# Performance work log

Measured on AMD Instinct MI355X. Metric: run time of the kernel, lower is better.

The kernel has to match this reference:

```python
import jax, jax.numpy as jnp
import numpy as np

N_PTS = 1048576
N_SPHERES = 128
K_SMOOTH = 32.0
CLAMP_MIN = 1e-6


def setup_inputs() -> dict:
    key = jax.random.key(0)
    k1, k2, k3 = jax.random.split(key, 3)
    p = jax.random.normal(k1, (N_PTS, 3), dtype=jnp.float32)
    centers = 0.3 * jax.random.uniform(k2, (N_SPHERES, 3), dtype=jnp.float32) - 0.15
    radii = 0.2 * jax.random.uniform(k3, (N_SPHERES,), dtype=jnp.float32) - 0.1
    tfs = jnp.zeros((N_SPHERES, 3, 3), dtype=jnp.float32)
    return {"p": p, "centers": centers, "radii": radii, "tfs": tfs}


def reference(p, centers, radii, tfs):
    # tfs + identity: per-sphere rigid-ish transform
    tfs_full = tfs + jnp.eye(3, dtype=tfs.dtype)  # [n, 3, 3]
    # q[i, b, :] = tfs_full[i] @ p[b] - centers[i]   -> [n, N, 3]
    q = jnp.einsum('ijk,bk->ibj', tfs_full, p) - centers[:, None, :]
    # signed distance to each sphere: [n, N]
    sd = jnp.linalg.norm(q, axis=-1) - radii[:, None]
    # smooth_min over sphere axis (dim 0), k=32
    s = jnp.sum(jnp.exp(-K_SMOOTH * sd), axis=0)  # [N]
    out = -jnp.log(jnp.clip(s, CLAMP_MIN)) / K_SMOOTH
    return out[..., None]  # [N, 1]
```

## Files before the change

kernel.cpp:

```cpp
#include <hip/hip_runtime.h>
#include <math.h>

#if __has_builtin(__builtin_amdgcn_exp2f)
#define EXP2F __builtin_amdgcn_exp2f
#else
#define EXP2F exp2f
#endif
#if __has_builtin(__builtin_amdgcn_logf)
#define LOG2FF __builtin_amdgcn_logf
#else
#define LOG2FF log2f
#endif
#if __has_builtin(__builtin_amdgcn_sqrtf)
#define SQRTFF __builtin_amdgcn_sqrtf
#else
#define SQRTFF sqrtf
#endif

#define K_SMOOTH 32.0f
#define LOG2E 1.4426950408889634f
#define LN2 0.6931471805599453f
#define CLAMP_MIN 1e-6f
#define FAR_OUT 0.43173470493638357f

constexpr int NS_MAX = 128;
constexpr int BLOCK = 256;
constexpr int CPTS = 4;
constexpr int PTS_PER_BLOCK = BLOCK * CPTS;

__global__ __launch_bounds__(BLOCK) void smoothed_spheres_kernel(
    const float* __restrict__ p, const float* __restrict__ centers,
    const float* __restrict__ radii, const float* __restrict__ tfs,
    float* __restrict__ out, int n_pts, int n_spheres) {
  __shared__ float4 sph_ce[NS_MAX];
  __shared__ float  sph_T[NS_MAX][9];
  __shared__ float4 queue[PTS_PER_BLOCK];
  __shared__ int    qcount;
  __shared__ float  redC[BLOCK / 64], redF[BLOCK / 64];
  __shared__ float  s_pthr2;
  __shared__ int    s_ident;

  const int tid = threadIdx.x;
  const int ns = (n_spheres < NS_MAX) ? n_spheres : NS_MAX;

  float candC = 0.0f;
  float candF = 0.0f;
  if (tid < ns) {
    const float cx = centers[3 * tid + 0];
    const float cy = centers[3 * tid + 1];
    const float cz = centers[3 * tid + 2];
    const float r = radii[tid];
    float fro = 0.0f;
#pragma unroll
    for (int j = 0; j < 9; ++j) {
      const float v = tfs[9 * tid + j];
      fro += v * v;
      sph_T[tid][j] = v + ((j == 0 || j == 4 || j == 8) ? 1.0f : 0.0f);
    }
    candC = SQRTFF(cx * cx + cy * cy + cz * cz) + r;
    candF = SQRTFF(fro);
    sph_ce[tid] = make_float4(cx, cy, cz, K_SMOOTH * LOG2E * r);
  }
  if (tid == 0) qcount = 0;

#pragma unroll
  for (int off = 32; off > 0; off >>= 1) {
    candC = fmaxf(candC, __shfl_xor(candC, off));
    candF = fmaxf(candF, __shfl_xor(candF, off));
  }
  if ((tid & 63) == 0) { redC[tid >> 6] = candC; redF[tid >> 6] = candF; }
  __syncthreads();
  if (tid == 0) {
    float Cmax = redC[0], Fmax = redF[0];
#pragma unroll
    for (int w = 1; w < BLOCK / 64; ++w) {
      Cmax = fmaxf(Cmax, redC[w]);
      Fmax = fmaxf(Fmax, redF[w]);
    }
    s_ident = (Fmax == 0.0f) ? 1 : 0;
    const float sd_req = logf((float)(ns > 0 ? ns : 1) * 1e6f) * (1.0f / K_SMOOTH) + 0.01f;
    if (Fmax < 1.0f) {
      const float pthr = (Cmax + sd_req) / (1.0f - Fmax);
      s_pthr2 = pthr * pthr;
    } else {
      s_pthr2 = 3.0e38f;
    }
  }
  __syncthreads();

  const int base = blockIdx.x * PTS_PER_BLOCK;
  const float pthr2 = s_pthr2;
#pragma unroll
  for (int j = 0; j < CPTS; ++j) {
    const int idx = base + j * BLOCK + tid;
    if (idx < n_pts) {
      const float px = p[3 * idx + 0];
      const float py = p[3 * idx + 1];
      const float pz = p[3 * idx + 2];
      const float pn2 = fmaf(px, px, fmaf(py, py, pz * pz));
      if (pn2 > pthr2) {
        out[idx] = FAR_OUT;
      } else {
        const int q = atomicAdd(&qcount, 1);
        queue[q] = make_float4(px, py, pz, __int_as_float(idx));
      }
    }
  }
  __syncthreads();
  const int qn = qcount;

  if (s_ident) {
    for (int qi = tid; qi < qn; qi += BLOCK) {
      const float4 e = queue[qi];
      const int idx = __float_as_int(e.w);
      const float px = e.x, py = e.y, pz = e.z;
      float s0 = 0.0f, s1 = 0.0f;
#pragma unroll 8
      for (int i = 0; i < ns; i += 2) {
        {
          const float4 c = sph_ce[i];
          const float dx = px - c.x;
          const float dy = py - c.y;
          const float dz = pz - c.z;
          const float d2 = fmaf(dx, dx, fmaf(dy, dy, dz * dz));
          s0 += EXP2F(fmaf(SQRTFF(d2), -K_SMOOTH * LOG2E, c.w));
        }
        {
          const float4 c = sph_ce[i + 1];
          const float dx = px - c.x;
          const float dy = py - c.y;
          const float dz = pz - c.z;
          const float d2 = fmaf(dx, dx, fmaf(dy, dy, dz * dz));
          s1 += EXP2F(fmaf(SQRTFF(d2), -K_SMOOTH * LOG2E, c.w));
        }
      }
      if (ns & 1) {
        const float4 c = sph_ce[ns - 1];
        const float dx = px - c.x;
        const float dy = py - c.y;
        const float dz = pz - c.z;
        const float d2 = fmaf(dx, dx, fmaf(dy, dy, dz * dz));
        s0 += EXP2F(fmaf(SQRTFF(d2), -K_SMOOTH * LOG2E, c.w));
      }
      const float s = fmaxf(s0 + s1, CLAMP_MIN);
      out[idx] = -LOG2FF(s) * (LN2 / K_SMOOTH);
    }
  } else {
    for (int qi = tid; qi < qn; qi += BLOCK) {
      const float4 e = queue[qi];
      const int idx = __float_as_int(e.w);
      const float px = e.x, py = e.y, pz = e.z;
      float s = 0.0f;
      for (int i = 0; i < ns; ++i) {
        const float4 c = sph_ce[i];
        const float* T = sph_T[i];
        const float qx = fmaf(T[0], px, fmaf(T[1], py, fmaf(T[2], pz, -c.x)));
        const float qy = fmaf(T[3], px, fmaf(T[4], py, fmaf(T[5], pz, -c.y)));
        const float qz = fmaf(T[6], px, fmaf(T[7], py, fmaf(T[8], pz, -c.z)));
        const float d2 = fmaf(qx, qx, fmaf(qy, qy, qz * qz));
        s += EXP2F(fmaf(SQRTFF(d2), -K_SMOOTH * LOG2E, c.w));
      }
      s = fmaxf(s, CLAMP_MIN);
      out[idx] = -LOG2FF(s) * (LN2 / K_SMOOTH);
    }
  }
}

extern "C" void kernel_launch(void* const* d_in, const int* in_sizes, int n_in,
                              void* d_out, int out_size, void* d_ws, size_t ws_size,
                              hipStream_t stream) {
  const float* p = (const float*)d_in[0];
  const float* centers = (const float*)d_in[1];
  const float* radii = (const float*)d_in[2];
  const float* tfs = (const float*)d_in[3];
  float* out = (float*)d_out;

  const int n_pts = in_sizes[0] / 3;
  const int n_spheres = in_sizes[2];

  const int grid = (n_pts + PTS_PER_BLOCK - 1) / PTS_PER_BLOCK;
  smoothed_spheres_kernel<<<grid, BLOCK, 0, stream>>>(p, centers, radii, tfs,
                                                      out, n_pts, n_spheres);
}
```

Before: 74.65 us.

## Split sphere loop across thread pairs and halve points per block

Each queued point is processed by two adjacent threads, each summing half of the spheres, and the partial sums are combined with a lane shuffle. Points per block are halved and a min-blocks hint is added to launch bounds to raise occupancy. This is meant to expose more parallelism and shorten per-thread chains, at the cost of an extra shuffle, a per-iteration bounds check and a possible register cap.

```diff
diff --git a/kernel.cpp b/kernel.cpp
--- a/kernel.cpp
+++ b/kernel.cpp
@@ -25,10 +25,10 @@
 
 constexpr int NS_MAX = 128;
 constexpr int BLOCK = 256;
-constexpr int CPTS = 4;
+constexpr int CPTS = 2;
 constexpr int PTS_PER_BLOCK = BLOCK * CPTS;
 
-__global__ __launch_bounds__(BLOCK) void smoothed_spheres_kernel(
+__global__ __launch_bounds__(BLOCK, 6) void smoothed_spheres_kernel(
     const float* __restrict__ p, const float* __restrict__ centers,
     const float* __restrict__ radii, const float* __restrict__ tfs,
     float* __restrict__ out, int n_pts, int n_spheres) {
@@ -110,23 +110,31 @@
   const int qn = qcount;
 
   if (s_ident) {
-    for (int qi = tid; qi < qn; qi += BLOCK) {
-      const float4 e = queue[qi];
-      const int idx = __float_as_int(e.w);
+    const int h = ns >> 1;
+    const int cntEven = h, cntOdd = ns - h;
+    const int total_w = 2 * qn;
+    for (int w0 = 0; w0 < total_w; w0 += BLOCK) {
+      const int w = w0 + tid;
+      const bool active = (w < total_w);
+      const int pt = active ? (w >> 1) : 0;
+      const float4 e = queue[pt];
       const float px = e.x, py = e.y, pz = e.z;
+      const int odd = w & 1;
+      const int start = odd ? h : 0;
+      const int cnt = odd ? cntOdd : cntEven;
       float s0 = 0.0f, s1 = 0.0f;
 #pragma unroll 8
-      for (int i = 0; i < ns; i += 2) {
+      for (int j = 0; j < cnt; j += 2) {
         {
-          const float4 c = sph_ce[i];
+          const float4 c = sph_ce[start + j];
           const float dx = px - c.x;
           const float dy = py - c.y;
           const float dz = pz - c.z;
           const float d2 = fmaf(dx, dx, fmaf(dy, dy, dz * dz));
           s0 += EXP2F(fmaf(SQRTFF(d2), -K_SMOOTH * LOG2E, c.w));
         }
-        {
-          const float4 c = sph_ce[i + 1];
+        if (j + 1 < cnt) {
+          const float4 c = sph_ce[start + j + 1];
           const float dx = px - c.x;
           const float dy = py - c.y;
           const float dz = pz - c.z;
@@ -134,16 +142,12 @@
           s1 += EXP2F(fmaf(SQRTFF(d2), -K_SMOOTH * LOG2E, c.w));
         }
       }
-      if (ns & 1) {
-        const float4 c = sph_ce[ns - 1];
-        const float dx = px - c.x;
-        const float dy = py - c.y;
-        const float dz = pz - c.z;
-        const float d2 = fmaf(dx, dx, fmaf(dy, dy, dz * dz));
-        s0 += EXP2F(fmaf(SQRTFF(d2), -K_SMOOTH * LOG2E, c.w));
+      float s = s0 + s1;
+      s += __shfl_xor(s, 1);
+      if (active && !odd) {
+        const float sc = fmaxf(s, CLAMP_MIN);
+        out[__float_as_int(e.w)] = -LOG2FF(sc) * (LN2 / K_SMOOTH);
       }
-      const float s = fmaxf(s0 + s1, CLAMP_MIN);
-      out[idx] = -LOG2FF(s) * (LN2 / K_SMOOTH);
     }
   } else {
     for (int qi = tid; qi < qn; qi += BLOCK) {
```

After: 78.02 us. +4.5%, slower.
